# Performance work log

Measured on AMD Instinct MI355X. Metric: run time of the kernel, lower is better.

The kernel has to match this reference:

```python
import jax, jax.numpy as jnp
import numpy as np

B, T, D = 4, 50, 512
SRC, SENTS, WORDS = 400, 16, 40
NEG = jnp.float32(-1e30)  # stands in for -inf mask fill (numerically identical post-softmax)


def _seq_mask(lengths, max_len):
    # [n, max_len] bool, True where position < length
    return jnp.arange(max_len)[None, :] < lengths[:, None]


def _mlp_score(q, h, Wq, bq, Uc, v):
    # Bahdanau additive score: v^T tanh(W q + U h)
    # q: [b,t,d], h: [b,s,d] -> [b,t,s]
    wq = q @ Wq + bq                       # [b,t,d]
    uh = h @ Uc                            # [b,s,d]
    wquh = jnp.tanh(wq[:, :, None, :] + uh[:, None, :, :])  # [b,t,s,d]
    return jnp.einsum('btsd,d->bts', wquh, v)


def setup_inputs() -> dict:
    key = jax.random.key(0)
    ks = jax.random.split(key, 20)
    s = np.float32(1.0 / np.sqrt(D))
    def p(k, shape):
        return jax.random.normal(k, shape, jnp.float32) * s
    return {
        'source': jax.random.normal(ks[0], (B, T, D), jnp.float32),
        'src_bank': jax.random.normal(ks[1], (SRC, B, D), jnp.float32),
        'src_lengths': jax.random.randint(ks[2], (B,), 1, SRC + 1),
        'qa_sent_bank': jax.random.normal(ks[3], (SENTS, B, D), jnp.float32),
        'qa_sent_lengths': jax.random.randint(ks[4], (B,), 1, SENTS + 1),
        'qa_word_bank': jax.random.normal(ks[5], (WORDS, B, SENTS, D), jnp.float32),
        'qa_word_lengths': jax.random.randint(ks[6], (B, SENTS), 1, WORDS + 1),
        'Wq_word': p(ks[7], (D, D)), 'bq_word': jnp.zeros((D,), jnp.float32),
        'Uc_word': p(ks[8], (D, D)), 'v_word': p(ks[9], (D,)),
        'Wq_sent': p(ks[10], (D, D)), 'bq_sent': jnp.zeros((D,), jnp.float32),
        'Uc_sent': p(ks[11], (D, D)), 'v_sent': p(ks[12], (D,)),
        'Wq_pass': p(ks[13], (D, D)), 'bq_pass': jnp.zeros((D,), jnp.float32),
        'Uc_pass': p(ks[14], (D, D)), 'v_pass': p(ks[15], (D,)),
    }


def _forward(source, src_bank, qa_sent_bank, qa_word_bank,
             Wq_word, bq_word, Uc_word, v_word,
             Wq_sent, bq_sent, Uc_sent, v_sent,
             Wq_pass, bq_pass, Uc_pass, v_pass,
             src_lengths, qa_word_lengths):
    b = source.shape[0]
    # [words,b,sents,d] -> [b,sents,words,d] -> [b, sents*words, d]
    qa_word = jnp.transpose(qa_word_bank, (1, 2, 0, 3)).reshape(b, SENTS * WORDS, D)
    src = jnp.transpose(src_bank, (1, 0, 2))       # [b,src,d]
    sent = jnp.transpose(qa_sent_bank, (1, 0, 2))  # [b,sents,d]

    qa_word_align = _mlp_score(source, qa_word, Wq_word, bq_word, Uc_word, v_word)  # [b,t,sents*words]
    src_align = _mlp_score(source, src, Wq_pass, bq_pass, Uc_pass, v_pass)          # [b,t,src]
    qa_sent_align = _mlp_score(source, sent, Wq_sent, bq_sent, Uc_sent, v_sent)     # [b,t,sents]

    # hierarchical combination: word score scaled by its sentence score
    qa_hier = (qa_word_align.reshape(b, T, SENTS, WORDS)
               * qa_sent_align[..., None]).reshape(b, T, SENTS * WORDS)

    align = jnp.concatenate([src_align, qa_hier], axis=-1)  # [b,t,src+sents*words]

    qa_mask = _seq_mask(qa_word_lengths.reshape(-1), WORDS).reshape(b, SENTS * WORDS)[:, None, :]
    src_mask = _seq_mask(src_lengths, SRC)[:, None, :]
    mask = jnp.concatenate([src_mask, qa_mask], axis=-1)

    align = jnp.where(mask, align, NEG)
    align_vectors = jax.nn.softmax(align, axis=-1)  # joint length-masked softmax

    memory = jnp.concatenate([src, qa_word], axis=1)          # [b, src+sents*words, d]
    c = jnp.einsum('bts,bsd->btd', align_vectors, memory)     # weighted context sum
    return c


def reference(source, src_bank, src_lengths, qa_sent_bank, qa_sent_lengths,
              qa_word_bank, qa_word_lengths,
              Wq_word, bq_word, Uc_word, v_word,
              Wq_sent, bq_sent, Uc_sent, v_sent,
              Wq_pass, bq_pass, Uc_pass, v_pass):
    # qa_sent_lengths is accepted but unused, matching the original forward()
    return _forward(source, src_bank, qa_sent_bank, qa_word_bank,
                    Wq_word, bq_word, Uc_word, v_word,
                    Wq_sent, bq_sent, Uc_sent, v_sent,
                    Wq_pass, bq_pass, Uc_pass, v_pass,
                    src_lengths, qa_word_lengths)
```

## Files before the change

### kernel.cpp

```cpp
#include <hip/hip_runtime.h>
#include <hip/hip_bf16.h>


#define B_    4
#define T_    50
#define D_    512
#define SRC_  400
#define SENTS_ 16
#define WORDS_ 40
#define NW_   640
#define NMEM_ 1040
#define NJOB_ 1056

#define C2L2E 2.8853900817779268f

typedef unsigned short ushort_t;
using s8v = __attribute__((ext_vector_type(8))) short;
using f4v = __attribute__((ext_vector_type(4))) float;

#define OFF_WQ_WORD 0
#define OFF_WQ_SENT 102400
#define OFF_WQ_PASS 204800
#define OFF_UH_SRC  307200
#define OFF_UH_WORD 1126400
#define OFF_UH_SENT 2437120
#define OFF_SC_SRC  2469888
#define OFF_SC_WORD 2549888
#define OFF_SC_SENT 2677888

__device__ __forceinline__ ushort_t f2b(float f) {
    __hip_bfloat16 h = __float2bfloat16(f);
    return *(ushort_t*)&h;
}

__global__ __launch_bounds__(256) void kA(
    const float* __restrict__ source, const float* __restrict__ src_bank,
    const float* __restrict__ qa_sent_bank, const float* __restrict__ qa_word_bank,
    const float* __restrict__ w0, const float* __restrict__ w1,
    const float* __restrict__ w2, const float* __restrict__ w3,
    const float* __restrict__ w4, const float* __restrict__ w5,
    const float* __restrict__ bq_word, const float* __restrict__ bq_sent,
    const float* __restrict__ bq_pass,
    float* __restrict__ wsf)
{
    __shared__ float smemf[4224];
    int bid = blockIdx.x;
    int tid = threadIdx.x;

    int z, rem;
    if (bid < 96)       { z = bid >> 5; rem = bid & 31; }
    else if (bid < 416) { z = 3; rem = bid - 96; }
    else if (bid < 616) { z = 4; rem = bid - 416; }
    else                { z = 5; rem = bid - 616; }
    int by = rem >> 3, bx = rem & 7;
    int M, atype; const float* bias; const float* W; float* C;
    switch (z) {
        case 0: M = 200;  atype = 0; bias = bq_word; W = w0; C = wsf + OFF_WQ_WORD; break;
        case 1: M = 200;  atype = 0; bias = bq_sent; W = w1; C = wsf + OFF_WQ_SENT; break;
        case 2: M = 200;  atype = 0; bias = bq_pass; W = w2; C = wsf + OFF_WQ_PASS; break;
        case 3: M = 2560; atype = 1; bias = nullptr; W = w3; C = wsf + OFF_UH_WORD; break;
        case 4: M = 1600; atype = 2; bias = nullptr; W = w4; C = wsf + OFF_UH_SRC;  break;
        default: M = 64;  atype = 3; bias = nullptr; W = w5; C = wsf + OFF_UH_SENT; break;
    }
    int m0 = by * 64, n0 = bx * 64;

    int lane = tid & 63, wvx = tid >> 6, quad = lane >> 4, l16 = lane & 15;
    int sm = tid >> 2, koff = (tid & 3) * 8;
    int rW = tid >> 3, cW = (tid & 7) * 8;
    int rWs = rW * 68 + (cW ^ (((rW >> 3) & 3) << 4));
    int nB = tid >> 2, kB8 = (tid & 3) * 8;
    int colp = nB ^ (((kB8 >> 3) & 3) << 4);

    short* At = (short*)smemf;
    short* Bt = (short*)(smemf + 1024);
    float* Wtmp = smemf + 2048;

    const float* arow = nullptr;
    {
        int rr = m0 + sm;
        if (rr < M) {
            if (atype == 0) arow = source + rr * D_;
            else if (atype == 1) { int b = rr / NW_; int j = rr - b * NW_;
                                   int se = j / WORDS_; int wd = j - se * WORDS_;
                                   arow = qa_word_bank + ((wd * B_ + b) * SENTS_ + se) * D_; }
            else if (atype == 2) { int b = rr / SRC_; int j = rr - b * SRC_;
                                   arow = src_bank + (j * B_ + b) * D_; }
            else                 { int b = rr >> 4; int s2 = rr & 15;
                                   arow = qa_sent_bank + (s2 * B_ + b) * D_; }
        }
    }
    const float* wbase = W + n0 + cW;

    auto loadA = [&](float* r, int kk) {
        if (arow) {
            float4 f0 = *(const float4*)(arow + kk * 32 + koff);
            float4 f1 = *(const float4*)(arow + kk * 32 + koff + 4);
            r[0]=f0.x; r[1]=f0.y; r[2]=f0.z; r[3]=f0.w;
            r[4]=f1.x; r[5]=f1.y; r[6]=f1.z; r[7]=f1.w;
        } else {
#pragma unroll
            for (int i = 0; i < 8; ++i) r[i] = 0.f;
        }
    };
    auto loadW = [&](float* r, int kk) {
        const float* p = wbase + (kk * 32 + rW) * D_;
        float4 f0 = *(const float4*)p;
        float4 f1 = *(const float4*)(p + 4);
        r[0]=f0.x; r[1]=f0.y; r[2]=f0.z; r[3]=f0.w;
        r[4]=f1.x; r[5]=f1.y; r[6]=f1.z; r[7]=f1.w;
    };
    auto storeWtmp = [&](const float* r) {
        *(float4*)(Wtmp + rWs)     = float4{r[0], r[1], r[2], r[3]};
        *(float4*)(Wtmp + rWs + 4) = float4{r[4], r[5], r[6], r[7]};
    };
    auto storeAt = [&](const float* r) {
        union { ushort_t u[8]; int4 v; } pk;
#pragma unroll
        for (int i = 0; i < 8; ++i) pk.u[i] = f2b(r[i]);
        *(int4*)(At + sm * 32 + koff) = pk.v;
    };
    auto buildBt = [&]() {
        union { ushort_t u[8]; int4 v; } pk;
#pragma unroll
        for (int i = 0; i < 8; ++i) pk.u[i] = f2b(Wtmp[(kB8 + i) * 68 + colp]);
        *(int4*)(Bt + nB * 32 + kB8) = pk.v;
    };

    f4v acc[4] = { {0.f,0.f,0.f,0.f}, {0.f,0.f,0.f,0.f},
                   {0.f,0.f,0.f,0.f}, {0.f,0.f,0.f,0.f} };

    float ac[8], an[8], wn[8];
    loadA(ac, 0);
    {
        float w0r[8];
        loadW(w0r, 0);
        storeWtmp(w0r);
    }
    loadW(wn, 1);
    loadA(an, 1);
    __syncthreads();

    for (int kk = 0; kk < 16; ++kk) {
        storeAt(ac);
        buildBt();
        __syncthreads();
        if (kk < 15) storeWtmp(wn);
        if (kk < 14) loadW(wn, kk + 2);
        if (kk < 15) {
#pragma unroll
            for (int i = 0; i < 8; ++i) ac[i] = an[i];
        }
        if (kk < 14) loadA(an, kk + 2);
        s8v af = *(const s8v*)(At + (wvx * 16 + l16) * 32 + quad * 8);
#pragma unroll
        for (int ng = 0; ng < 4; ++ng) {
            s8v bf = *(const s8v*)(Bt + (ng * 16 + l16) * 32 + quad * 8);
            acc[ng] = __builtin_amdgcn_mfma_f32_16x16x32_bf16(af, bf, acc[ng], 0, 0, 0);
        }
        __syncthreads();
    }

#pragma unroll
    for (int ng = 0; ng < 4; ++ng) {
        int col = n0 + ng * 16 + l16;
        float bb = bias ? bias[col] : 0.f;
#pragma unroll
        for (int rr2 = 0; rr2 < 4; ++rr2) {
            int row = m0 + wvx * 16 + quad * 4 + rr2;
            if (row < M) C[row * D_ + col] = (acc[ng][rr2] + bb) * C2L2E;
        }
    }
}

__global__ __launch_bounds__(256) void k2_scores(
    const float* __restrict__ v_word, const float* __restrict__ v_sent,
    const float* __restrict__ v_pass,
    const int* __restrict__ src_lengths, const int* __restrict__ qa_word_lengths,
    float* __restrict__ wsf)
{
    int lane = threadIdx.x & 63;
    int jid = blockIdx.x * 4 + (threadIdx.x >> 6);
    int job = jid / 5, fifth = jid - job * 5;
    int b = job / NJOB_, slot = job - b * NJOB_;
    const float* uh; const float* v; const float* wq; float* out; int ostride;
    if (slot < SRC_) {
        if (slot >= src_lengths[b]) return;
        uh = wsf + OFF_UH_SRC + (size_t)(b * SRC_ + slot) * D_;
        v = v_pass; wq = wsf + OFF_WQ_PASS + b * T_ * D_;
        out = wsf + OFF_SC_SRC + b * T_ * SRC_ + slot; ostride = SRC_;
    } else if (slot < NMEM_) {
        int j = slot - SRC_;
        int se = j / WORDS_; int wd = j - se * WORDS_;
        if (wd >= qa_word_lengths[b * SENTS_ + se]) return;
        uh = wsf + OFF_UH_WORD + (size_t)(b * NW_ + j) * D_;
        v = v_word; wq = wsf + OFF_WQ_WORD + b * T_ * D_;
        out = wsf + OFF_SC_WORD + b * T_ * NW_ + j; ostride = NW_;
    } else {
        int s2 = slot - NMEM_;
        uh = wsf + OFF_UH_SENT + (size_t)(b * SENTS_ + s2) * D_;
        v = v_sent; wq = wsf + OFF_WQ_SENT + b * T_ * D_;
        out = wsf + OFF_SC_SENT + b * T_ * SENTS_ + s2; ostride = SENTS_;
    }
    int d0 = lane * 8;
    float4 u0 = *(const float4*)(uh + d0);
    float4 u1 = *(const float4*)(uh + d0 + 4);
    float uhr[8] = {u0.x, u0.y, u0.z, u0.w, u1.x, u1.y, u1.z, u1.w};
    float4 v0 = *(const float4*)(v + d0);
    float4 v1 = *(const float4*)(v + d0 + 4);
    float vr[8] = {v0.x, v0.y, v0.z, v0.w, v1.x, v1.y, v1.z, v1.w};

    float vs = ((vr[0] + vr[1]) + (vr[2] + vr[3])) + ((vr[4] + vr[5]) + (vr[6] + vr[7]));
#pragma unroll
    for (int off = 32; off > 0; off >>= 1) vs += __shfl_xor(vs, off, 64);

    const float* wqh = wq + (fifth * 10) * D_ + d0;
    int tbase = fifth * 10;
#pragma unroll 1
    for (int g = 0; g < 2; ++g) {
        float a5[5];
#pragma unroll
        for (int u5 = 0; u5 < 5; ++u5) {
            const float* wr = wqh + (g * 5 + u5) * D_;
            float4 w0 = *(const float4*)(wr);
            float4 w1 = *(const float4*)(wr + 4);
            float wrr[8] = {w0.x, w0.y, w0.z, w0.w, w1.x, w1.y, w1.z, w1.w};
            float a = 0.f;
#pragma unroll
            for (int j = 0; j < 8; ++j) {
                float e = __builtin_amdgcn_exp2f(wrr[j] + uhr[j]);
                float r = __builtin_amdgcn_rcpf(e + 1.f);
                a = fmaf(vr[j], r, a);
            }
            a5[u5] = a;
        }
#pragma unroll
        for (int off = 32; off > 0; off >>= 1) {
#pragma unroll
            for (int u5 = 0; u5 < 5; ++u5) a5[u5] += __shfl_xor(a5[u5], off, 64);
        }
        if (lane == 0) {
#pragma unroll
            for (int u5 = 0; u5 < 5; ++u5)
                out[(tbase + g * 5 + u5) * ostride] = fmaf(-2.f, a5[u5], vs);
        }
    }
}

__global__ __launch_bounds__(256) void k3ac(
    const int* __restrict__ src_lengths, const int* __restrict__ qa_word_lengths,
    const float* __restrict__ wsf,
    const float* __restrict__ src_bank, const float* __restrict__ qa_word_bank,
    float* __restrict__ out)
{
    __shared__ float p[NMEM_];
    __shared__ float part[256];
    __shared__ float red[4];
    int tid = threadIdx.x, lane = tid & 63, wv = tid >> 6;
    int bid = blockIdx.x;
    int bt = bid >> 2, dq = bid & 3;
    int b = bt / T_, t = bt - b * T_;
    const float* sc_src  = wsf + OFF_SC_SRC  + bt * SRC_;
    const float* sc_word = wsf + OFF_SC_WORD + bt * NW_;
    const float* sc_sent = wsf + OFF_SC_SENT + bt * SENTS_;
    int slen = src_lengths[b];

    float mx = -3.0e38f;
    for (int j = tid; j < NMEM_; j += 256) {
        float val;
        if (j < SRC_) {
            val = (j < slen) ? sc_src[j] : -1e30f;
        } else {
            int jj = j - SRC_; int se = jj / WORDS_; int wd = jj - se * WORDS_;
            float raw = sc_word[jj] * sc_sent[se];
            val = (wd < qa_word_lengths[b * SENTS_ + se]) ? raw : -1e30f;
        }
        p[j] = val;
        mx = fmaxf(mx, val);
    }
#pragma unroll
    for (int off = 32; off > 0; off >>= 1) mx = fmaxf(mx, __shfl_xor(mx, off, 64));
    if (lane == 0) red[wv] = mx;
    __syncthreads();
    mx = fmaxf(fmaxf(red[0], red[1]), fmaxf(red[2], red[3]));
    __syncthreads();
    float lsum = 0.f;
    for (int j = tid; j < NMEM_; j += 256) {
        float e = __expf(p[j] - mx);
        p[j] = e; lsum += e;
    }
#pragma unroll
    for (int off = 32; off > 0; off >>= 1) lsum += __shfl_xor(lsum, off, 64);
    if (lane == 0) red[wv] = lsum;
    __syncthreads();
    float inv = 1.f / (red[0] + red[1] + red[2] + red[3]);
    for (int j = tid; j < NMEM_; j += 256) p[j] *= inv;
    __syncthreads();

    int c = tid & 127, sh = tid >> 7;
    int d = dq * 128 + c;
    float acc = 0.f;

    auto gemv8 = [&](const float* bank, int strd, const float* pseg, int r0, int r1) {
        if (r0 >= r1) return;
        const float* rp = bank + (size_t)r0 * strd;
        float m0 = rp[0], m1 = rp[strd], m2 = rp[2*strd], m3 = rp[3*strd];
        float m4 = rp[4*strd], m5 = rp[5*strd], m6 = rp[6*strd], m7 = rp[7*strd];
        float4 pa = *(const float4*)(pseg + r0);
        float4 pb = *(const float4*)(pseg + r0 + 4);
        for (int r = r0; r + 8 < r1; r += 8) {
            const float* np = bank + (size_t)(r + 8) * strd;
            float n0 = np[0], n1 = np[strd], n2 = np[2*strd], n3 = np[3*strd];
            float n4 = np[4*strd], n5 = np[5*strd], n6 = np[6*strd], n7 = np[7*strd];
            float4 qa = *(const float4*)(pseg + r + 8);
            float4 qb = *(const float4*)(pseg + r + 12);
            acc = fmaf(pa.x, m0, acc); acc = fmaf(pa.y, m1, acc);
            acc = fmaf(pa.z, m2, acc); acc = fmaf(pa.w, m3, acc);
            acc = fmaf(pb.x, m4, acc); acc = fmaf(pb.y, m5, acc);
            acc = fmaf(pb.z, m6, acc); acc = fmaf(pb.w, m7, acc);
            m0 = n0; m1 = n1; m2 = n2; m3 = n3;
            m4 = n4; m5 = n5; m6 = n6; m7 = n7;
            pa = qa; pb = qb;
        }
        acc = fmaf(pa.x, m0, acc); acc = fmaf(pa.y, m1, acc);
        acc = fmaf(pa.z, m2, acc); acc = fmaf(pa.w, m3, acc);
        acc = fmaf(pb.x, m4, acc); acc = fmaf(pb.y, m5, acc);
        acc = fmaf(pb.z, m6, acc); acc = fmaf(pb.w, m7, acc);
    };

    {
        int slen8 = (slen + 7) & ~7;
        const float* bank = src_bank + (size_t)b * D_ + d;
        int s0 = (sh == 0) ? 0 : 200;
        int s1 = (sh == 0) ? min(slen8, 200) : slen8;
        gemv8(bank, B_ * D_, p, s0, s1);
    }
#pragma unroll 1
    for (int se = sh * 8; se < sh * 8 + 8; ++se) {
        int lim = qa_word_lengths[b * SENTS_ + se];
        int lim8 = (lim + 7) & ~7;
        const float* bank = qa_word_bank + ((size_t)b * SENTS_ + se) * D_ + d;
        gemv8(bank, B_ * SENTS_ * D_, p + SRC_ + se * WORDS_, 0, lim8);
    }

    part[tid] = acc;
    __syncthreads();
    if (tid < 128)
        out[(size_t)(b * T_ + t) * D_ + dq * 128 + tid] = part[tid] + part[tid + 128];
}

extern "C" void kernel_launch(void* const* d_in, const int* in_sizes, int n_in,
                              void* d_out, int out_size, void* d_ws, size_t ws_size,
                              hipStream_t stream)
{
    (void)in_sizes; (void)n_in; (void)out_size; (void)ws_size;
    const float* source          = (const float*)d_in[0];
    const float* src_bank        = (const float*)d_in[1];
    const int*   src_lengths     = (const int*)d_in[2];
    const float* qa_sent_bank    = (const float*)d_in[3];
    const float* qa_word_bank    = (const float*)d_in[5];
    const int*   qa_word_lengths = (const int*)d_in[6];
    const float* Wq_word = (const float*)d_in[7];
    const float* bq_word = (const float*)d_in[8];
    const float* Uc_word = (const float*)d_in[9];
    const float* v_word  = (const float*)d_in[10];
    const float* Wq_sent = (const float*)d_in[11];
    const float* bq_sent = (const float*)d_in[12];
    const float* Uc_sent = (const float*)d_in[13];
    const float* v_sent  = (const float*)d_in[14];
    const float* Wq_pass = (const float*)d_in[15];
    const float* bq_pass = (const float*)d_in[16];
    const float* Uc_pass = (const float*)d_in[17];
    const float* v_pass  = (const float*)d_in[18];

    float* wsf = (float*)d_ws;
    float* out = (float*)d_out;

    kA<<<dim3(624), dim3(256), 0, stream>>>(
        source, src_bank, qa_sent_bank, qa_word_bank,
        Wq_word, Wq_sent, Wq_pass, Uc_word, Uc_pass, Uc_sent,
        bq_word, bq_sent, bq_pass, wsf);
    k2_scores<<<dim3(5280), dim3(256), 0, stream>>>(
        v_word, v_sent, v_pass, src_lengths, qa_word_lengths, wsf);
    k3ac<<<dim3(800), dim3(256), 0, stream>>>(
        src_lengths, qa_word_lengths, wsf, src_bank, qa_word_bank, out);
}
```

Baseline: 159.4 us.

## Pair memory slots per wave in score kernel and widen context kernel to 512 threads

The score kernel now has each wave handle two adjacent memory slots, so every loaded Wq row is reused for two tanh/dot evaluations. This halves the grid and the Wq traffic per score, at the cost of more registers and partial work on odd-length tails. The context kernel moves from 256 to 512 threads per block, splitting the weighted-sum rows four ways instead of two to add memory-level parallelism. The four partial sums are then reduced in shared memory.

```diff
diff --git a/kernel.cpp b/kernel.cpp
--- a/kernel.cpp
+++ b/kernel.cpp
@@ -10,7 +10,6 @@
 #define WORDS_ 40
 #define NW_   640
 #define NMEM_ 1040
-#define NJOB_ 1056
 
 #define C2L2E 2.8853900817779268f
 
@@ -181,30 +180,42 @@
     int lane = threadIdx.x & 63;
     int jid = blockIdx.x * 4 + (threadIdx.x >> 6);
     int job = jid / 5, fifth = jid - job * 5;
-    int b = job / NJOB_, slot = job - b * NJOB_;
+    int b = job / 528, pair = job - b * 528;
     const float* uh; const float* v; const float* wq; float* out; int ostride;
-    if (slot < SRC_) {
-        if (slot >= src_lengths[b]) return;
-        uh = wsf + OFF_UH_SRC + (size_t)(b * SRC_ + slot) * D_;
+    int nact;
+    if (pair < 200) {
+        int slot0 = pair * 2;
+        int slen = src_lengths[b];
+        if (slot0 >= slen) return;
+        nact = min(2, slen - slot0);
+        uh = wsf + OFF_UH_SRC + (size_t)(b * SRC_ + slot0) * D_;
         v = v_pass; wq = wsf + OFF_WQ_PASS + b * T_ * D_;
-        out = wsf + OFF_SC_SRC + b * T_ * SRC_ + slot; ostride = SRC_;
-    } else if (slot < NMEM_) {
-        int j = slot - SRC_;
-        int se = j / WORDS_; int wd = j - se * WORDS_;
-        if (wd >= qa_word_lengths[b * SENTS_ + se]) return;
-        uh = wsf + OFF_UH_WORD + (size_t)(b * NW_ + j) * D_;
+        out = wsf + OFF_SC_SRC + b * T_ * SRC_ + slot0; ostride = SRC_;
+    } else if (pair < 520) {
+        int jw = (pair - 200) * 2;
+        int se = jw / WORDS_; int wd = jw - se * WORDS_;
+        int lim = qa_word_lengths[b * SENTS_ + se];
+        if (wd >= lim) return;
+        nact = min(2, lim - wd);
+        uh = wsf + OFF_UH_WORD + (size_t)(b * NW_ + jw) * D_;
         v = v_word; wq = wsf + OFF_WQ_WORD + b * T_ * D_;
-        out = wsf + OFF_SC_WORD + b * T_ * NW_ + j; ostride = NW_;
+        out = wsf + OFF_SC_WORD + b * T_ * NW_ + jw; ostride = NW_;
     } else {
-        int s2 = slot - NMEM_;
+        int s2 = (pair - 520) * 2;
+        nact = 2;
         uh = wsf + OFF_UH_SENT + (size_t)(b * SENTS_ + s2) * D_;
         v = v_sent; wq = wsf + OFF_WQ_SENT + b * T_ * D_;
         out = wsf + OFF_SC_SENT + b * T_ * SENTS_ + s2; ostride = SENTS_;
     }
     int d0 = lane * 8;
-    float4 u0 = *(const float4*)(uh + d0);
-    float4 u1 = *(const float4*)(uh + d0 + 4);
-    float uhr[8] = {u0.x, u0.y, u0.z, u0.w, u1.x, u1.y, u1.z, u1.w};
+    float uhr[2][8];
+#pragma unroll
+    for (int u = 0; u < 2; ++u) {
+        float4 f0 = *(const float4*)(uh + u * D_ + d0);
+        float4 f1 = *(const float4*)(uh + u * D_ + d0 + 4);
+        uhr[u][0]=f0.x; uhr[u][1]=f0.y; uhr[u][2]=f0.z; uhr[u][3]=f0.w;
+        uhr[u][4]=f1.x; uhr[u][5]=f1.y; uhr[u][6]=f1.z; uhr[u][7]=f1.w;
+    }
     float4 v0 = *(const float4*)(v + d0);
     float4 v1 = *(const float4*)(v + d0 + 4);
     float vr[8] = {v0.x, v0.y, v0.z, v0.w, v1.x, v1.y, v1.z, v1.w};
@@ -217,44 +228,54 @@
     int tbase = fifth * 10;
 #pragma unroll 1
     for (int g = 0; g < 2; ++g) {
-        float a5[5];
+        float a[2][5];
 #pragma unroll
         for (int u5 = 0; u5 < 5; ++u5) {
             const float* wr = wqh + (g * 5 + u5) * D_;
             float4 w0 = *(const float4*)(wr);
             float4 w1 = *(const float4*)(wr + 4);
             float wrr[8] = {w0.x, w0.y, w0.z, w0.w, w1.x, w1.y, w1.z, w1.w};
-            float a = 0.f;
-#pragma unroll
-            for (int j = 0; j < 8; ++j) {
-                float e = __builtin_amdgcn_exp2f(wrr[j] + uhr[j]);
-                float r = __builtin_amdgcn_rcpf(e + 1.f);
-                a = fmaf(vr[j], r, a);
+#pragma unroll
+            for (int u = 0; u < 2; ++u) {
+                float acc = 0.f;
+#pragma unroll
+                for (int j = 0; j < 8; ++j) {
+                    float e = __builtin_amdgcn_exp2f(wrr[j] + uhr[u][j]);
+                    float rc = __builtin_amdgcn_rcpf(e + 1.f);
+                    acc = fmaf(vr[j], rc, acc);
+                }
+                a[u][u5] = acc;
             }
-            a5[u5] = a;
         }
 #pragma unroll
         for (int off = 32; off > 0; off >>= 1) {
 #pragma unroll
-            for (int u5 = 0; u5 < 5; ++u5) a5[u5] += __shfl_xor(a5[u5], off, 64);
+            for (int u = 0; u < 2; ++u)
+#pragma unroll
+                for (int u5 = 0; u5 < 5; ++u5)
+                    a[u][u5] += __shfl_xor(a[u][u5], off, 64);
         }
         if (lane == 0) {
 #pragma unroll
-            for (int u5 = 0; u5 < 5; ++u5)
-                out[(tbase + g * 5 + u5) * ostride] = fmaf(-2.f, a5[u5], vs);
+            for (int u5 = 0; u5 < 5; ++u5) {
+                int trow = (tbase + g * 5 + u5) * ostride;
+#pragma unroll
+                for (int u = 0; u < 2; ++u)
+                    if (u < nact) out[trow + u] = fmaf(-2.f, a[u][u5], vs);
+            }
         }
     }
 }
 
-__global__ __launch_bounds__(256) void k3ac(
+__global__ __launch_bounds__(512) void k3ac(
     const int* __restrict__ src_lengths, const int* __restrict__ qa_word_lengths,
     const float* __restrict__ wsf,
     const float* __restrict__ src_bank, const float* __restrict__ qa_word_bank,
     float* __restrict__ out)
 {
     __shared__ float p[NMEM_];
-    __shared__ float part[256];
-    __shared__ float red[4];
+    __shared__ float part[512];
+    __shared__ float red[8];
     int tid = threadIdx.x, lane = tid & 63, wv = tid >> 6;
     int bid = blockIdx.x;
     int bt = bid >> 2, dq = bid & 3;
@@ -265,7 +286,7 @@
     int slen = src_lengths[b];
 
     float mx = -3.0e38f;
-    for (int j = tid; j < NMEM_; j += 256) {
+    for (int j = tid; j < NMEM_; j += 512) {
         float val;
         if (j < SRC_) {
             val = (j < slen) ? sc_src[j] : -1e30f;
@@ -281,10 +302,11 @@
     for (int off = 32; off > 0; off >>= 1) mx = fmaxf(mx, __shfl_xor(mx, off, 64));
     if (lane == 0) red[wv] = mx;
     __syncthreads();
-    mx = fmaxf(fmaxf(red[0], red[1]), fmaxf(red[2], red[3]));
+    mx = fmaxf(fmaxf(fmaxf(red[0], red[1]), fmaxf(red[2], red[3])),
+               fmaxf(fmaxf(red[4], red[5]), fmaxf(red[6], red[7])));
     __syncthreads();
     float lsum = 0.f;
-    for (int j = tid; j < NMEM_; j += 256) {
+    for (int j = tid; j < NMEM_; j += 512) {
         float e = __expf(p[j] - mx);
         p[j] = e; lsum += e;
     }
@@ -292,11 +314,12 @@
     for (int off = 32; off > 0; off >>= 1) lsum += __shfl_xor(lsum, off, 64);
     if (lane == 0) red[wv] = lsum;
     __syncthreads();
-    float inv = 1.f / (red[0] + red[1] + red[2] + red[3]);
-    for (int j = tid; j < NMEM_; j += 256) p[j] *= inv;
-    __syncthreads();
-
-    int c = tid & 127, sh = tid >> 7;
+    float inv = 1.f / (((red[0] + red[1]) + (red[2] + red[3])) +
+                       ((red[4] + red[5]) + (red[6] + red[7])));
+    for (int j = tid; j < NMEM_; j += 512) p[j] *= inv;
+    __syncthreads();
+
+    int c = tid & 127, sq = tid >> 7;
     int d = dq * 128 + c;
     float acc = 0.f;
 
@@ -330,12 +353,12 @@
     {
         int slen8 = (slen + 7) & ~7;
         const float* bank = src_bank + (size_t)b * D_ + d;
-        int s0 = (sh == 0) ? 0 : 200;
-        int s1 = (sh == 0) ? min(slen8, 200) : slen8;
-        gemv8(bank, B_ * D_, p, s0, s1);
+        int r0 = sq * 104;
+        int r1 = min(slen8, r0 + 104);
+        gemv8(bank, B_ * D_, p, r0, r1);
     }
 #pragma unroll 1
-    for (int se = sh * 8; se < sh * 8 + 8; ++se) {
+    for (int se = sq * 4; se < sq * 4 + 4; ++se) {
         int lim = qa_word_lengths[b * SENTS_ + se];
         int lim8 = (lim + 7) & ~7;
         const float* bank = qa_word_bank + ((size_t)b * SENTS_ + se) * D_ + d;
@@ -345,7 +368,8 @@
     part[tid] = acc;
     __syncthreads();
     if (tid < 128)
-        out[(size_t)(b * T_ + t) * D_ + dq * 128 + tid] = part[tid] + part[tid + 128];
+        out[(size_t)(b * T_ + t) * D_ + dq * 128 + tid] =
+            (part[tid] + part[tid + 128]) + (part[tid + 256] + part[tid + 384]);
 }
 
 extern "C" void kernel_launch(void* const* d_in, const int* in_sizes, int n_in,
@@ -379,8 +403,8 @@
         source, src_bank, qa_sent_bank, qa_word_bank,
         Wq_word, Wq_sent, Wq_pass, Uc_word, Uc_pass, Uc_sent,
         bq_word, bq_sent, bq_pass, wsf);
-    k2_scores<<<dim3(5280), dim3(256), 0, stream>>>(
+    k2_scores<<<dim3(2640), dim3(256), 0, stream>>>(
         v_word, v_sent, v_pass, src_lengths, qa_word_lengths, wsf);
-    k3ac<<<dim3(800), dim3(256), 0, stream>>>(
+    k3ac<<<dim3(800), dim3(512), 0, stream>>>(
         src_lengths, qa_word_lengths, wsf, src_bank, qa_word_bank, out);
 }
```

Result: no change. 159.8 us (+0.3%).
